# Kernel tuning notes

Measured on AMD Instinct MI355X. Metric: run time of the kernel, lower is better.

Reference implementation:

```python
import jax, jax.numpy as jnp
import numpy as np

B, S, D, H = 4, 2048, 1024, 16
HD = D // H  # head size = 64


def setup_inputs() -> dict:
    key = jax.random.key(0)
    ks = jax.random.split(key, 8)
    scale = 1.0 / np.sqrt(D)
    return {
        "q": jax.random.normal(ks[0], (B, S, D), jnp.float32),
        "k": jax.random.normal(ks[1], (B, S, D), jnp.float32),
        "v": jax.random.normal(ks[2], (B, S, D), jnp.float32),
        "mask": jnp.ones((B, 1, S), dtype=bool),
        "Wq": jax.random.normal(ks[3], (D, D), jnp.float32) * scale,
        "bq": jnp.zeros((D,), jnp.float32),
        "Wk": jax.random.normal(ks[4], (D, D), jnp.float32) * scale,
        "bk": jnp.zeros((D,), jnp.float32),
        "Wv": jax.random.normal(ks[5], (D, D), jnp.float32) * scale,
        "bv": jnp.zeros((D,), jnp.float32),
        "Wo": jax.random.normal(ks[6], (D, D), jnp.float32) * scale,
        "bo": jnp.zeros((D,), jnp.float32),
    }


def _split_heads(x):
    # [B, S, D] -> [B, H, S, HD]
    return x.reshape(B, -1, H, HD).transpose(0, 2, 1, 3)


def reference(q, k, v, mask, Wq, bq, Wk, bk, Wv, bv, Wo, bo):
    qh = _split_heads(q @ Wq + bq) / jnp.sqrt(jnp.asarray(HD, q.dtype))
    kh = _split_heads(k @ Wk + bk)
    vh = _split_heads(v @ Wv + bv)
    # scores: [B, H, Sq, Sk]
    scores = jnp.einsum("bhqd,bhkd->bhqk", qh, kh)
    neg_inf = jnp.asarray(-jnp.inf, scores.dtype)
    scores = jnp.where(mask[:, None, :, :], scores, neg_inf)
    attn = jax.nn.softmax(scores, axis=-1)
    # dropout p=0.0 -> identity (eval semantics)
    ctx = jnp.einsum("bhqk,bhkd->bhqd", attn, vh)
    ctx = ctx.transpose(0, 2, 1, 3).reshape(B, -1, D)
    return ctx @ Wo + bo
```

## Files before the change

### kernel.cpp

```cpp
#include <hip/hip_runtime.h>
#include <hip/hip_bf16.h>


typedef __bf16 bf16_t;
typedef __bf16 bf16x8 __attribute__((ext_vector_type(8)));
typedef __bf16 bf16x4 __attribute__((ext_vector_type(4)));
typedef float  floatx4 __attribute__((ext_vector_type(4)));

constexpr int B_ = 4, S_ = 2048, D_ = 1024, H_ = 16, HD_ = 64;
constexpr int M_ = B_ * S_;

#if defined(__has_builtin)
#if __has_builtin(__builtin_amdgcn_exp2f)
#define EXP2_RAW __builtin_amdgcn_exp2f
#endif
#endif
#ifndef EXP2_RAW
#define EXP2_RAW __builtin_exp2f
#endif

__device__ __forceinline__ void gll16(const void* gsrc, void* ldst) {
  __builtin_amdgcn_global_load_lds(
      (__attribute__((address_space(1))) void*)gsrc,
      (__attribute__((address_space(3))) void*)ldst, 16, 0, 0);
}

struct WPtrs { const float* src[4]; bf16_t* dst[4]; };

__global__ __launch_bounds__(256)
void transpose_cast_w(WPtrs p) {
  __shared__ float tile[64][65];
  const int m  = blockIdx.y;
  const int kt = blockIdx.x >> 4;
  const int nt = blockIdx.x & 15;
  const float* W  = p.src[m];
  bf16_t*      Wt = p.dst[m];
  const int t = threadIdx.x;
#pragma unroll
  for (int i = 0; i < 16; ++i) {
    int idx = i*256 + t;
    int r = idx >> 6, c = idx & 63;
    tile[r][c] = W[(kt*64 + r)*D_ + nt*64 + c];
  }
  __syncthreads();
#pragma unroll
  for (int i = 0; i < 16; ++i) {
    int idx = i*256 + t;
    int r = idx >> 6, c = idx & 63;
    Wt[(long)(nt*64 + r)*D_ + kt*64 + c] = (bf16_t)tile[c][r];
  }
}

struct ProjArgs {
  const float*  A[3];
  const bf16_t* Bt[3];
  const float*  bias[3];
  float         scale[3];
  void*         out[3];
  int           epi[3];
};

__global__ __launch_bounds__(256)
void proj_gemm(ProjArgs pa) {
  __shared__ alignas(16) bf16_t AsT[128*72];
  __shared__ alignas(16) char   Bs[128*64*2];

  const int z    = blockIdx.z;
  const int tid  = threadIdx.x;
  const int lane = tid & 63;
  const int w    = tid >> 6;
  const int quad = lane >> 4;
  const int l16  = lane & 15;
  const int wr   = w >> 1, wc = w & 1;
  const long row0 = (long)blockIdx.x * 128;
  const int  col0 = blockIdx.y * 128;

  const float*  A  = pa.A[z];
  const bf16_t* Bt = pa.Bt[z];

  floatx4 acc[4][4];
#pragma unroll
  for (int i = 0; i < 4; ++i)
#pragma unroll
    for (int j = 0; j < 4; ++j) { floatx4 zz = {0.f,0.f,0.f,0.f}; acc[i][j] = zz; }

  for (int kt = 0; kt < D_/64; ++kt) {
    const int k0 = kt * 64;
#pragma unroll
    for (int i = 0; i < 8; ++i) {
      int g = i*256 + tid;
      int r = g >> 4, c4 = g & 15;
      float4 f = *(const float4*)(A + (row0 + r)*D_ + k0 + c4*4);
      bf16x4 pk;
      pk[0]=(bf16_t)f.x; pk[1]=(bf16_t)f.y; pk[2]=(bf16_t)f.z; pk[3]=(bf16_t)f.w;
      *(bf16x4*)(AsT + r*72 + c4*4) = pk;
    }
#pragma unroll
    for (int it = 0; it < 4; ++it) {
      int chunk = it*4 + w;
      int g = chunk*64 + lane;
      int r = g >> 3, cs = g & 7;
      int cg = cs ^ (r & 7);
      gll16(Bt + (long)(col0 + r)*D_ + k0 + cg*8, Bs + chunk*1024);
    }
    __syncthreads();

#pragma unroll
    for (int ks = 0; ks < 2; ++ks) {
      bf16x8 a[4], b[4];
#pragma unroll
      for (int i = 0; i < 4; ++i) {
        int r = wr*64 + i*16 + l16;
        a[i] = *(const bf16x8*)(AsT + r*72 + (ks*4 + quad)*8);
      }
#pragma unroll
      for (int j = 0; j < 4; ++j) {
        int r = wc*64 + j*16 + l16;
        int c = ks*4 + quad;
        b[j] = *(const bf16x8*)(Bs + ((r*8) + (c ^ (r & 7)))*16);
      }
#pragma unroll
      for (int i = 0; i < 4; ++i)
#pragma unroll
        for (int j = 0; j < 4; ++j)
          acc[i][j] = __builtin_amdgcn_mfma_f32_16x16x32_bf16(a[i], b[j], acc[i][j], 0, 0, 0);
    }
    __syncthreads();
  }

  const float* bias = pa.bias[z];
  const float scale = pa.scale[z];
  if (pa.epi[z] == 0) {
    bf16_t* C = (bf16_t*)pa.out[z];
#pragma unroll
    for (int j = 0; j < 4; ++j) {
      int c = col0 + wc*64 + j*16 + l16;
      float bv = bias[c];
#pragma unroll
      for (int i = 0; i < 4; ++i) {
        long r = row0 + wr*64 + i*16 + quad*4;
#pragma unroll
        for (int rg = 0; rg < 4; ++rg)
          C[(r+rg)*D_ + c] = (bf16_t)((acc[i][j][rg] + bv) * scale);
      }
    }
  } else {
    bf16_t* VT = (bf16_t*)pa.out[z];
#pragma unroll
    for (int j = 0; j < 4; ++j) {
      int c  = col0 + wc*64 + j*16 + l16;
      int h  = c >> 6, hd = c & 63;
      float bv = bias[c];
#pragma unroll
      for (int i = 0; i < 4; ++i) {
        long r = row0 + wr*64 + i*16 + quad*4;
        int b = (int)(r >> 11), s = (int)(r & 2047);
        bf16x4 pk;
#pragma unroll
        for (int rg = 0; rg < 4; ++rg) pk[rg] = (bf16_t)(acc[i][j][rg] + bv);
        *(bf16x4*)(VT + ((long)((b*H_ + h)*HD_ + hd))*S_ + s) = pk;
      }
    }
  }
}

__global__ __launch_bounds__(256)
void out_gemm(const bf16_t* __restrict__ Ap, const bf16_t* __restrict__ Bt,
              const float* __restrict__ bias, float* __restrict__ Cp)
{
  __shared__ alignas(16) char smem[128*64*2 + 128*64*2];
  char* As = smem;
  char* Bs = smem + 128*64*2;

  const int tid  = threadIdx.x;
  const int lane = tid & 63;
  const int w    = tid >> 6;
  const int quad = lane >> 4;
  const int l16  = lane & 15;
  const int wr   = w >> 1, wc = w & 1;
  const long row0 = (long)blockIdx.x * 128;
  const int  col0 = blockIdx.y * 128;

  floatx4 acc[4][4];
#pragma unroll
  for (int i = 0; i < 4; ++i)
#pragma unroll
    for (int j = 0; j < 4; ++j) { floatx4 zz = {0.f,0.f,0.f,0.f}; acc[i][j] = zz; }

  for (int kt = 0; kt < D_/64; ++kt) {
    const int k0 = kt * 64;
#pragma unroll
    for (int it = 0; it < 4; ++it) {
      int chunk = it*4 + w;
      int g = chunk*64 + lane;
      int r = g >> 3, cs = g & 7;
      int cg = cs ^ (r & 7);
      gll16(Ap + (long)(row0 + r)*D_ + k0 + cg*8, As + chunk*1024);
    }
#pragma unroll
    for (int it = 0; it < 4; ++it) {
      int chunk = it*4 + w;
      int g = chunk*64 + lane;
      int r = g >> 3, cs = g & 7;
      int cg = cs ^ (r & 7);
      gll16(Bt + (long)(col0 + r)*D_ + k0 + cg*8, Bs + chunk*1024);
    }
    __syncthreads();

#pragma unroll
    for (int ks = 0; ks < 2; ++ks) {
      bf16x8 a[4], b[4];
#pragma unroll
      for (int i = 0; i < 4; ++i) {
        int r = wr*64 + i*16 + l16;
        int c = ks*4 + quad;
        a[i] = *(const bf16x8*)(As + ((r*8) + (c ^ (r & 7)))*16);
      }
#pragma unroll
      for (int j = 0; j < 4; ++j) {
        int r = wc*64 + j*16 + l16;
        int c = ks*4 + quad;
        b[j] = *(const bf16x8*)(Bs + ((r*8) + (c ^ (r & 7)))*16);
      }
#pragma unroll
      for (int i = 0; i < 4; ++i)
#pragma unroll
        for (int j = 0; j < 4; ++j)
          acc[i][j] = __builtin_amdgcn_mfma_f32_16x16x32_bf16(a[i], b[j], acc[i][j], 0, 0, 0);
    }
    __syncthreads();
  }

#pragma unroll
  for (int j = 0; j < 4; ++j) {
    int c = col0 + wc*64 + j*16 + l16;
    float bv = bias[c];
#pragma unroll
    for (int i = 0; i < 4; ++i) {
      long r = row0 + wr*64 + i*16 + quad*4;
#pragma unroll
      for (int rg = 0; rg < 4; ++rg)
        Cp[(r+rg)*D_ + c] = acc[i][j][rg] + bv;
    }
  }
}

__global__ __launch_bounds__(256, 2)
void attn(const bf16_t* __restrict__ Qp, const bf16_t* __restrict__ Kp,
          const bf16_t* __restrict__ VTg, bf16_t* __restrict__ Ctx)
{
  __shared__ alignas(16) bf16_t Ks [2][128*64];
  __shared__ alignas(16) bf16_t VTs[2][64*128];
  __shared__ alignas(16) bf16_t Ps [4][32*64];

  const int tid  = threadIdx.x;
  const int lane = tid & 63;
  const int w    = tid >> 6;
  const int quad = lane >> 4;
  const int l16  = lane & 15;

  const int h  = blockIdx.x;
  const int qt = blockIdx.y;
  const int b  = blockIdx.z;
  const int bh = b*H_ + h;
  const long rowQ0 = (long)b * S_ + qt*128;
  const int  colH  = h * HD_;

  bf16x8 qf[2][2];
#pragma unroll
  for (int ks = 0; ks < 2; ++ks)
#pragma unroll
    for (int qs = 0; qs < 2; ++qs)
      qf[ks][qs] = *(const bf16x8*)(Qp + (rowQ0 + w*32 + qs*16 + l16)*D_ + colH + ks*32 + quad*8);

  floatx4 O[4][2];
#pragma unroll
  for (int vb = 0; vb < 4; ++vb)
#pragma unroll
    for (int qs = 0; qs < 2; ++qs) { floatx4 zz = {0.f,0.f,0.f,0.f}; O[vb][qs] = zz; }
  float lsum[2] = {0.f, 0.f};

  bf16_t* Pw = &Ps[w][0];

  {
    const long rowK0 = (long)b * S_;
#pragma unroll
    for (int i = 0; i < 4; ++i) {
      int chunk = w*4 + i;
      int G = chunk*64 + lane;
      int r = G >> 3, cs = G & 7, cg = cs ^ (r & 7);
      gll16(Kp + (rowK0 + r)*D_ + colH + cg*8, (char*)Ks[0] + chunk*1024);
    }
#pragma unroll
    for (int i = 0; i < 4; ++i) {
      int chunk = w*4 + i;
      int G = chunk*64 + lane;
      int r = G >> 4, cs = G & 15, cg = cs ^ (r & 15);
      gll16(VTg + ((long)(bh*HD_ + r))*S_ + cg*8, (char*)VTs[0] + chunk*1024);
    }
  }

  for (int kt = 0; kt < S_/128; ++kt) {
    __syncthreads();
    const int bs = kt & 1;

    if (kt + 1 < S_/128) {
      const int  kn    = kt + 1, bn = kn & 1;
      const int  kv0n  = kn*128;
      const long rowK0 = (long)b * S_ + kv0n;
#pragma unroll
      for (int i = 0; i < 4; ++i) {
        int chunk = w*4 + i;
        int G = chunk*64 + lane;
        int r = G >> 3, cs = G & 7, cg = cs ^ (r & 7);
        gll16(Kp + (rowK0 + r)*D_ + colH + cg*8, (char*)Ks[bn] + chunk*1024);
      }
#pragma unroll
      for (int i = 0; i < 4; ++i) {
        int chunk = w*4 + i;
        int G = chunk*64 + lane;
        int r = G >> 4, cs = G & 15, cg = cs ^ (r & 15);
        gll16(VTg + ((long)(bh*HD_ + r))*S_ + kv0n + cg*8, (char*)VTs[bn] + chunk*1024);
      }
    }

    floatx4 sc[8][2];
#pragma unroll
    for (int nb = 0; nb < 8; ++nb)
#pragma unroll
      for (int qs = 0; qs < 2; ++qs) { floatx4 zz = {0.f,0.f,0.f,0.f}; sc[nb][qs] = zz; }
#pragma unroll
    for (int ks = 0; ks < 2; ++ks) {
#pragma unroll
      for (int nb = 0; nb < 8; ++nb) {
        bf16x8 a = *(const bf16x8*)(Ks[bs] + (nb*16 + l16)*64 + (((ks*4 + quad) ^ (l16 & 7))*8));
#pragma unroll
        for (int qs = 0; qs < 2; ++qs)
          sc[nb][qs] = __builtin_amdgcn_mfma_f32_16x16x32_bf16(a, qf[ks][qs], sc[nb][qs], 0, 0, 0);
      }
    }

#pragma unroll
    for (int half = 0; half < 2; ++half) {
#pragma unroll
      for (int nbl = 0; nbl < 4; ++nbl) {
        int nb = half*4 + nbl;
#pragma unroll
        for (int qs = 0; qs < 2; ++qs) {
          bf16x4 pk;
#pragma unroll
          for (int rg = 0; rg < 4; ++rg) {
            float p = EXP2_RAW(sc[nb][qs][rg]);
            lsum[qs] += p;
            pk[rg] = (bf16_t)p;
          }
          *(bf16x4*)(Pw + (qs*16 + l16)*64 + ((2*nbl + (quad >> 1)) ^ (l16 & 7))*8 + (quad & 1)*4) = pk;
        }
      }
#pragma unroll
      for (int kbl = 0; kbl < 2; ++kbl) {
        bf16x8 pf[2];
#pragma unroll
        for (int qs = 0; qs < 2; ++qs)
          pf[qs] = *(const bf16x8*)(Pw + (qs*16 + l16)*64 + (((kbl*4 + quad) ^ (l16 & 7))*8));
#pragma unroll
        for (int vb = 0; vb < 4; ++vb) {
          bf16x8 vf = *(const bf16x8*)(VTs[bs] + (vb*16 + l16)*128 + (((half*8 + kbl*4 + quad) ^ l16)*8));
#pragma unroll
          for (int qs = 0; qs < 2; ++qs)
            O[vb][qs] = __builtin_amdgcn_mfma_f32_16x16x32_bf16(pf[qs], vf, O[vb][qs], 0, 0, 0);
        }
      }
    }
  }

#pragma unroll
  for (int qs = 0; qs < 2; ++qs) {
    lsum[qs] += __shfl_xor(lsum[qs], 16);
    lsum[qs] += __shfl_xor(lsum[qs], 32);
  }
#pragma unroll
  for (int qs = 0; qs < 2; ++qs)
#pragma unroll
    for (int rg = 0; rg < 4; ++rg) {
      float lv  = __shfl(lsum[qs], (lane & 48) | (quad*4 + rg));
      float inv = 1.0f / lv;
      long  r   = rowQ0 + w*32 + qs*16 + quad*4 + rg;
#pragma unroll
      for (int vb = 0; vb < 4; ++vb)
        Ctx[r*D_ + colH + vb*16 + l16] = (bf16_t)(O[vb][qs][rg] * inv);
    }
}

extern "C" void kernel_launch(void* const* d_in, const int* in_sizes, int n_in,
                              void* d_out, int out_size, void* d_ws, size_t ws_size,
                              hipStream_t stream)
{
  (void)in_sizes; (void)n_in; (void)out_size; (void)ws_size;
  const float* q  = (const float*)d_in[0];
  const float* k  = (const float*)d_in[1];
  const float* v  = (const float*)d_in[2];
  const float* Wq = (const float*)d_in[4];
  const float* bq = (const float*)d_in[5];
  const float* Wk = (const float*)d_in[6];
  const float* bk = (const float*)d_in[7];
  const float* Wv = (const float*)d_in[8];
  const float* bv = (const float*)d_in[9];
  const float* Wo = (const float*)d_in[10];
  const float* bo = (const float*)d_in[11];

  char* ws = (char*)d_ws;
  bf16_t* WTq = (bf16_t*)(ws + ((size_t)0 << 20));
  bf16_t* WTk = (bf16_t*)(ws + ((size_t)2 << 20));
  bf16_t* WTv = (bf16_t*)(ws + ((size_t)4 << 20));
  bf16_t* WTo = (bf16_t*)(ws + ((size_t)6 << 20));
  bf16_t* QP  = (bf16_t*)(ws + ((size_t)8  << 20));
  bf16_t* KP  = (bf16_t*)(ws + ((size_t)24 << 20));
  bf16_t* VTg = (bf16_t*)(ws + ((size_t)40 << 20));
  bf16_t* CTX = (bf16_t*)(ws + ((size_t)56 << 20));

  WPtrs wp;
  wp.src[0] = Wq; wp.src[1] = Wk; wp.src[2] = Wv; wp.src[3] = Wo;
  wp.dst[0] = WTq; wp.dst[1] = WTk; wp.dst[2] = WTv; wp.dst[3] = WTo;
  transpose_cast_w<<<dim3(256, 4), 256, 0, stream>>>(wp);

  ProjArgs pa;
  pa.A[0] = q;  pa.A[1] = k;  pa.A[2] = v;
  pa.Bt[0] = WTq; pa.Bt[1] = WTk; pa.Bt[2] = WTv;
  pa.bias[0] = bq; pa.bias[1] = bk; pa.bias[2] = bv;
  pa.scale[0] = 1.4426950408889634f / 8.0f;
  pa.scale[1] = 1.0f; pa.scale[2] = 1.0f;
  pa.out[0] = QP; pa.out[1] = KP; pa.out[2] = VTg;
  pa.epi[0] = 0; pa.epi[1] = 0; pa.epi[2] = 1;
  proj_gemm<<<dim3(M_/128, D_/128, 3), 256, 0, stream>>>(pa);

  attn<<<dim3(H_, S_/128, B_), 256, 0, stream>>>(QP, KP, VTg, CTX);

  out_gemm<<<dim3(M_/128, D_/128), 256, 0, stream>>>(CTX, WTo, bo, (float*)d_out);
}
```

Before: 348.9 us.

## Double-buffer projection and output GEMMs and shrink output tile width

Adds double-buffered LDS for the QKV projection and output GEMMs. The next K-tile is prefetched (A through registers with the bf16 cast, B through direct global-to-LDS loads) while the current tile feeds the MFMAs, which also removes one barrier per iteration. The projection A tile moves to the XOR-swizzled layout. The output GEMM tile shrinks to 128x64 to double the block count and improve CU occupancy. The trade-off is more LDS and registers per block and more redundant A loads in the output GEMM.

Result: slower. 367.5 us (+5.3%).

```diff
diff --git a/kernel.cpp b/kernel.cpp
--- a/kernel.cpp
+++ b/kernel.cpp
@@ -61,9 +61,9 @@
 };
 
 __global__ __launch_bounds__(256)
-void proj_gemm(ProjArgs pa) {
-  __shared__ alignas(16) bf16_t AsT[128*72];
-  __shared__ alignas(16) char   Bs[128*64*2];
+void proj_gemm_fused(ProjArgs pa) {
+  __shared__ alignas(16) char As[2][128*64*2];
+  __shared__ alignas(16) char Bs[2][128*64*2];
 
   const int z    = blockIdx.z;
   const int tid  = threadIdx.x;
@@ -78,32 +78,54 @@
   const float*  A  = pa.A[z];
   const bf16_t* Bt = pa.Bt[z];
 
+  const int ar = tid >> 4;
+  const int ac4 = tid & 15;
+  const int acs = ac4 >> 1, ahf = ac4 & 1;
+
   floatx4 acc[4][4];
 #pragma unroll
   for (int i = 0; i < 4; ++i)
 #pragma unroll
     for (int j = 0; j < 4; ++j) { floatx4 zz = {0.f,0.f,0.f,0.f}; acc[i][j] = zz; }
 
+  float4 areg[8];
+
+#pragma unroll
+  for (int it = 0; it < 4; ++it) {
+    int chunk = it*4 + w;
+    int g = chunk*64 + lane;
+    int r = g >> 3, cs = g & 7, cg = cs ^ (r & 7);
+    gll16(Bt + (long)(col0 + r)*D_ + 0 + cg*8, Bs[0] + chunk*1024);
+  }
+#pragma unroll
+  for (int i = 0; i < 8; ++i)
+    areg[i] = *(const float4*)(A + (row0 + i*16 + ar)*D_ + 0 + ac4*4);
+#pragma unroll
+  for (int i = 0; i < 8; ++i) {
+    bf16x4 pk;
+    pk[0]=(bf16_t)areg[i].x; pk[1]=(bf16_t)areg[i].y;
+    pk[2]=(bf16_t)areg[i].z; pk[3]=(bf16_t)areg[i].w;
+    int rr = i*16 + ar;
+    *(bf16x4*)(As[0] + ((rr*8 + (acs ^ (rr & 7)))*16 + ahf*8)) = pk;
+  }
+
   for (int kt = 0; kt < D_/64; ++kt) {
-    const int k0 = kt * 64;
-#pragma unroll
-    for (int i = 0; i < 8; ++i) {
-      int g = i*256 + tid;
-      int r = g >> 4, c4 = g & 15;
-      float4 f = *(const float4*)(A + (row0 + r)*D_ + k0 + c4*4);
-      bf16x4 pk;
-      pk[0]=(bf16_t)f.x; pk[1]=(bf16_t)f.y; pk[2]=(bf16_t)f.z; pk[3]=(bf16_t)f.w;
-      *(bf16x4*)(AsT + r*72 + c4*4) = pk;
-    }
-#pragma unroll
-    for (int it = 0; it < 4; ++it) {
-      int chunk = it*4 + w;
-      int g = chunk*64 + lane;
-      int r = g >> 3, cs = g & 7;
-      int cg = cs ^ (r & 7);
-      gll16(Bt + (long)(col0 + r)*D_ + k0 + cg*8, Bs + chunk*1024);
-    }
+    const int c = kt & 1;
     __syncthreads();
+
+    if (kt + 1 < D_/64) {
+      const int k0n = (kt + 1) * 64;
+#pragma unroll
+      for (int it = 0; it < 4; ++it) {
+        int chunk = it*4 + w;
+        int g = chunk*64 + lane;
+        int r = g >> 3, cs = g & 7, cg = cs ^ (r & 7);
+        gll16(Bt + (long)(col0 + r)*D_ + k0n + cg*8, Bs[c^1] + chunk*1024);
+      }
+#pragma unroll
+      for (int i = 0; i < 8; ++i)
+        areg[i] = *(const float4*)(A + (row0 + i*16 + ar)*D_ + k0n + ac4*4);
+    }
 
 #pragma unroll
     for (int ks = 0; ks < 2; ++ks) {
@@ -111,13 +133,14 @@
 #pragma unroll
       for (int i = 0; i < 4; ++i) {
         int r = wr*64 + i*16 + l16;
-        a[i] = *(const bf16x8*)(AsT + r*72 + (ks*4 + quad)*8);
+        int cc = ks*4 + quad;
+        a[i] = *(const bf16x8*)(As[c] + ((r*8) + (cc ^ (r & 7)))*16);
       }
 #pragma unroll
       for (int j = 0; j < 4; ++j) {
         int r = wc*64 + j*16 + l16;
-        int c = ks*4 + quad;
-        b[j] = *(const bf16x8*)(Bs + ((r*8) + (c ^ (r & 7)))*16);
+        int cc = ks*4 + quad;
+        b[j] = *(const bf16x8*)(Bs[c] + ((r*8) + (cc ^ (r & 7)))*16);
       }
 #pragma unroll
       for (int i = 0; i < 4; ++i)
@@ -125,7 +148,17 @@
         for (int j = 0; j < 4; ++j)
           acc[i][j] = __builtin_amdgcn_mfma_f32_16x16x32_bf16(a[i], b[j], acc[i][j], 0, 0, 0);
     }
-    __syncthreads();
+
+    if (kt + 1 < D_/64) {
+#pragma unroll
+      for (int i = 0; i < 8; ++i) {
+        bf16x4 pk;
+        pk[0]=(bf16_t)areg[i].x; pk[1]=(bf16_t)areg[i].y;
+        pk[2]=(bf16_t)areg[i].z; pk[3]=(bf16_t)areg[i].w;
+        int rr = i*16 + ar;
+        *(bf16x4*)(As[c^1] + ((rr*8 + (acs ^ (rr & 7)))*16 + ahf*8)) = pk;
+      }
+    }
   }
 
   const float* bias = pa.bias[z];
@@ -168,79 +201,93 @@
 void out_gemm(const bf16_t* __restrict__ Ap, const bf16_t* __restrict__ Bt,
               const float* __restrict__ bias, float* __restrict__ Cp)
 {
-  __shared__ alignas(16) char smem[128*64*2 + 128*64*2];
-  char* As = smem;
-  char* Bs = smem + 128*64*2;
+  __shared__ alignas(16) char As[2][128*64*2];
+  __shared__ alignas(16) char Bs[2][64*64*2];
 
   const int tid  = threadIdx.x;
   const int lane = tid & 63;
   const int w    = tid >> 6;
   const int quad = lane >> 4;
   const int l16  = lane & 15;
-  const int wr   = w >> 1, wc = w & 1;
   const long row0 = (long)blockIdx.x * 128;
-  const int  col0 = blockIdx.y * 128;
-
-  floatx4 acc[4][4];
-#pragma unroll
-  for (int i = 0; i < 4; ++i)
+  const int  col0 = blockIdx.y * 64;
+
+  floatx4 acc[2][4];
+#pragma unroll
+  for (int i = 0; i < 2; ++i)
 #pragma unroll
     for (int j = 0; j < 4; ++j) { floatx4 zz = {0.f,0.f,0.f,0.f}; acc[i][j] = zz; }
 
+#pragma unroll
+  for (int it = 0; it < 4; ++it) {
+    int chunk = it*4 + w;
+    int g = chunk*64 + lane;
+    int r = g >> 3, cs = g & 7, cg = cs ^ (r & 7);
+    gll16(Ap + (long)(row0 + r)*D_ + cg*8, As[0] + chunk*1024);
+  }
+#pragma unroll
+  for (int it = 0; it < 2; ++it) {
+    int chunk = it*4 + w;
+    int g = chunk*64 + lane;
+    int r = g >> 3, cs = g & 7, cg = cs ^ (r & 7);
+    gll16(Bt + (long)(col0 + r)*D_ + cg*8, Bs[0] + chunk*1024);
+  }
+
   for (int kt = 0; kt < D_/64; ++kt) {
-    const int k0 = kt * 64;
-#pragma unroll
-    for (int it = 0; it < 4; ++it) {
-      int chunk = it*4 + w;
-      int g = chunk*64 + lane;
-      int r = g >> 3, cs = g & 7;
-      int cg = cs ^ (r & 7);
-      gll16(Ap + (long)(row0 + r)*D_ + k0 + cg*8, As + chunk*1024);
-    }
-#pragma unroll
-    for (int it = 0; it < 4; ++it) {
-      int chunk = it*4 + w;
-      int g = chunk*64 + lane;
-      int r = g >> 3, cs = g & 7;
-      int cg = cs ^ (r & 7);
-      gll16(Bt + (long)(col0 + r)*D_ + k0 + cg*8, Bs + chunk*1024);
-    }
+    const int c = kt & 1;
     __syncthreads();
 
+    if (kt + 1 < D_/64) {
+      const int k0n = (kt + 1) * 64;
+#pragma unroll
+      for (int it = 0; it < 4; ++it) {
+        int chunk = it*4 + w;
+        int g = chunk*64 + lane;
+        int r = g >> 3, cs = g & 7, cg = cs ^ (r & 7);
+        gll16(Ap + (long)(row0 + r)*D_ + k0n + cg*8, As[c^1] + chunk*1024);
+      }
+#pragma unroll
+      for (int it = 0; it < 2; ++it) {
+        int chunk = it*4 + w;
+        int g = chunk*64 + lane;
+        int r = g >> 3, cs = g & 7, cg = cs ^ (r & 7);
+        gll16(Bt + (long)(col0 + r)*D_ + k0n + cg*8, Bs[c^1] + chunk*1024);
+      }
+    }
+
 #pragma unroll
     for (int ks = 0; ks < 2; ++ks) {
-      bf16x8 a[4], b[4];
-#pragma unroll
-      for (int i = 0; i < 4; ++i) {
-        int r = wr*64 + i*16 + l16;
-        int c = ks*4 + quad;
-        a[i] = *(const bf16x8*)(As + ((r*8) + (c ^ (r & 7)))*16);
+      bf16x8 a[2], b[4];
+#pragma unroll
+      for (int i = 0; i < 2; ++i) {
+        int r = w*32 + i*16 + l16;
+        int cc = ks*4 + quad;
+        a[i] = *(const bf16x8*)(As[c] + ((r*8) + (cc ^ (r & 7)))*16);
       }
 #pragma unroll
       for (int j = 0; j < 4; ++j) {
-        int r = wc*64 + j*16 + l16;
-        int c = ks*4 + quad;
-        b[j] = *(const bf16x8*)(Bs + ((r*8) + (c ^ (r & 7)))*16);
-      }
-#pragma unroll
-      for (int i = 0; i < 4; ++i)
+        int r = j*16 + l16;
+        int cc = ks*4 + quad;
+        b[j] = *(const bf16x8*)(Bs[c] + ((r*8) + (cc ^ (r & 7)))*16);
+      }
+#pragma unroll
+      for (int i = 0; i < 2; ++i)
 #pragma unroll
         for (int j = 0; j < 4; ++j)
           acc[i][j] = __builtin_amdgcn_mfma_f32_16x16x32_bf16(a[i], b[j], acc[i][j], 0, 0, 0);
     }
-    __syncthreads();
   }
 
 #pragma unroll
   for (int j = 0; j < 4; ++j) {
-    int c = col0 + wc*64 + j*16 + l16;
-    float bv = bias[c];
-#pragma unroll
-    for (int i = 0; i < 4; ++i) {
-      long r = row0 + wr*64 + i*16 + quad*4;
+    int cc = col0 + j*16 + l16;
+    float bv = bias[cc];
+#pragma unroll
+    for (int i = 0; i < 2; ++i) {
+      long r = row0 + w*32 + i*16 + quad*4;
 #pragma unroll
       for (int rg = 0; rg < 4; ++rg)
-        Cp[(r+rg)*D_ + c] = acc[i][j][rg] + bv;
+        Cp[(r+rg)*D_ + cc] = acc[i][j][rg] + bv;
     }
   }
 }
@@ -432,9 +479,9 @@
   pa.scale[1] = 1.0f; pa.scale[2] = 1.0f;
   pa.out[0] = QP; pa.out[1] = KP; pa.out[2] = VTg;
   pa.epi[0] = 0; pa.epi[1] = 0; pa.epi[2] = 1;
-  proj_gemm<<<dim3(M_/128, D_/128, 3), 256, 0, stream>>>(pa);
+  proj_gemm_fused<<<dim3(M_/128, D_/128, 3), 256, 0, stream>>>(pa);
 
   attn<<<dim3(H_, S_/128, B_), 256, 0, stream>>>(QP, KP, VTg, CTX);
 
-  out_gemm<<<dim3(M_/128, D_/128), 256, 0, stream>>>(CTX, WTo, bo, (float*)d_out);
-}
+  out_gemm<<<dim3(M_/128, D_/64), 256, 0, stream>>>(CTX, WTo, bo, (float*)d_out);
+}
```
